# Kernel tuning notes

Measured on AMD Instinct MI355X. Metric: run time of the kernel, lower is better.

Reference implementation:

```python
import jax, jax.numpy as jnp
import numpy as np

NUM_LEVELS = 2
RADIUS = 3


def setup_inputs() -> dict:
    key = jax.random.key(0)
    k1, k2, k3 = jax.random.split(key, 3)
    x = jax.random.normal(k1, (4, 320, 9, 32, 32), dtype=jnp.float32)
    w_fc0 = jax.random.normal(k2, (160, 320), dtype=jnp.float32) * 0.05
    w_fc1 = jax.random.normal(k3, (160, 320), dtype=jnp.float32) * 0.05
    return {"x": x, "w_fc0": w_fc0, "w_fc1": w_fc1}


def _bilinear_zeros(img, xs, ys):
    # img: (M, H, W); xs, ys: (M, K) pixel coords.
    # Matches F.grid_sample(mode='bilinear', padding_mode='zeros', align_corners=True):
    # align_corners normalization round-trips to the raw pixel coords, and
    # out-of-bounds corners contribute zero.
    M, H, W = img.shape
    x0f = jnp.floor(xs)
    y0f = jnp.floor(ys)
    wx = xs - x0f
    wy = ys - y0f
    x0 = x0f.astype(jnp.int32)
    y0 = y0f.astype(jnp.int32)
    x1 = x0 + 1
    y1 = y0 + 1
    n = jnp.arange(M)[:, None]

    def corner(yi, xi):
        valid = (xi >= 0) & (xi < W) & (yi >= 0) & (yi < H)
        v = img[n, jnp.clip(yi, 0, H - 1), jnp.clip(xi, 0, W - 1)]
        return v * valid.astype(img.dtype)

    v00 = corner(y0, x0)
    v01 = corner(y0, x1)
    v10 = corner(y1, x0)
    v11 = corner(y1, x1)
    return (v00 * (1 - wx) * (1 - wy) + v01 * wx * (1 - wy)
            + v10 * (1 - wx) * wy + v11 * wx * wy)


def reference(x, w_fc0, w_fc1):
    b, c, T, h, w = x.shape
    xt = jnp.transpose(x, (0, 2, 1, 3, 4))  # (b, T, c, h, w)
    # 1x1 convs (no bias) on consecutive-frame pairs
    f0 = jnp.einsum('btchw,oc->bothw', xt[:, :-1], w_fc0)
    f1 = jnp.einsum('btchw,oc->bothw', xt[:, 1:], w_fc1)
    t = T - 1
    c2 = w_fc0.shape[0]
    f0 = f0.reshape(b * t, c2, h * w)
    f1 = f1.reshape(b * t, c2, h * w)
    # all-pairs correlation volume, normalized by channel count
    corr = jnp.einsum('nci,ncj->nij', f0, f1) / c2  # (bt, hw, hw)
    corr = corr.reshape(b * t * h * w, h, w)

    # pyramid via 2x2 avg pooling
    pyramid = [corr]
    for _ in range(NUM_LEVELS - 1):
        M, H, W = pyramid[-1].shape
        pyramid.append(pyramid[-1].reshape(M, H // 2, 2, W // 2, 2).mean(axis=(2, 4)))

    # per-pixel centroids (x, y), tiled over the bt batch axis
    ys, xs = jnp.meshgrid(jnp.arange(h), jnp.arange(w), indexing='ij')
    cx = jnp.tile(xs.reshape(-1).astype(jnp.float32), b * t)  # (bt*h*w,)
    cy = jnp.tile(ys.reshape(-1).astype(jnp.float32), b * t)

    # delta[i, j] = (d[i], d[j]); delta[...,0] -> x offset, delta[...,1] -> y offset
    r = RADIUS
    d = jnp.linspace(-r, r, 2 * r + 1)
    dx = jnp.repeat(d, 2 * r + 1)  # varies along first window dim
    dy = jnp.tile(d, 2 * r + 1)    # varies along second window dim

    outs = []
    for i, ci in enumerate(pyramid):
        xs_s = cx[:, None] / (2 ** i) + dx[None, :]  # (M, K)
        ys_s = cy[:, None] / (2 ** i) + dy[None, :]
        v = _bilinear_zeros(ci, xs_s, ys_s)          # (M, (2r+1)^2)
        outs.append(v.reshape(b * t, h, w, -1))
    out = jnp.concatenate(outs, axis=3)              # (bt, h, w, L*(2r+1)^2)
    out = out.reshape(b, t, h, w, -1)
    return jnp.transpose(out, (0, 4, 1, 2, 3)).astype(jnp.float32)
```

## Files before the change

kernel.cpp:

```cpp
#include <hip/hip_runtime.h>
#include <hip/hip_bf16.h>

typedef __attribute__((ext_vector_type(8))) short short8;
typedef __attribute__((ext_vector_type(4))) float f32x4;

static constexpr int HW = 1024;
static constexpr int C2 = 160;
static constexpr int FS = 168;
static constexpr int FSC = 160;
static constexpr int KSTEPS = 10;
static constexpr size_t PL = 32ull * 1024 * 160;
static constexpr size_t PPL = 32ull * 256 * 160;
static constexpr int AIMG = 6656;

__device__ inline short bfh(float v) {
  __hip_bfloat16 h = __float2bfloat16(v);
  return *reinterpret_cast<short*>(&h);
}
__device__ inline float bff(short s) {
  union { unsigned u; float f; } c;
  c.u = ((unsigned)(unsigned short)s) << 16;
  return c.f;
}

typedef const __attribute__((address_space(1))) void* gas_t;
typedef __attribute__((address_space(3))) void* las_t;
__device__ inline void gload_lds16(const void* g, void* l) {
  __builtin_amdgcn_global_load_lds((gas_t)g, (las_t)l, 16, 0, 0);
}

__global__ __launch_bounds__(256)
void wprep2_kernel(const float* __restrict__ w0, const float* __restrict__ w1,
                   short* __restrict__ wp) {
  const int id = blockIdx.x * 256 + threadIdx.x;
  if (id >= KSTEPS * 4 * AIMG) return;
  const int img = id / AIMG, r = id % AIMG;
  const int ks = img >> 2, qp = img & 3;
  short outv = 0;
  if (r < 6400) {
    const int hl = r / 3200;
    const int g2 = r % 3200;
    const int gr = g2 / 40, kk = g2 % 40;
    const int mat = gr >= 40;
    const int o = qp * 40 + gr - mat * 40;
    if (kk < 32) {
      const float v = (mat ? w1 : w0)[o * 320 + ks * 32 + kk];
      const short hb = bfh(v);
      outv = hl ? bfh(v - bff(hb)) : hb;
    }
  }
  wp[id] = outv;
}

__global__ __launch_bounds__(256)
void conv_fused(const float* __restrict__ x, const short* __restrict__ wprep2,
                short* __restrict__ f0bh, short* __restrict__ f0bl,
                short* __restrict__ f1bh, short* __restrict__ f1bl) {
  __shared__ __align__(16) char lds[31744];
  float* xF = reinterpret_cast<float*>(lds);
  short* aL = reinterpret_cast<short*>(lds + 18432);
  short* tL = reinterpret_cast<short*>(lds);

  const int flat = blockIdx.x;
  const int xcd = flat & 7;
  const int mem = (flat >> 3) & 7;
  const int qp = mem >> 1;
  const int pxh = mem & 1;
  const int g = (flat >> 6) * 8 + xcd;
  const int bb = g >> 5;
  const int pxt = (g & 31) * 2 + pxh;
  const int tid = threadIdx.x;
  const int lane = tid & 63;
  const int wave = __builtin_amdgcn_readfirstlane(tid >> 6);
  const int lr = lane & 15, kg = lane >> 4;

  f32x4 acc[5][3];
#pragma unroll
  for (int mt = 0; mt < 5; ++mt)
#pragma unroll
    for (int fi = 0; fi < 3; ++fi)
#pragma unroll
      for (int r = 0; r < 4; ++r) acc[mt][fi][r] = 0.f;

  const float* xg = x + ((size_t)(bb * 320) * 9) * 1024 + (size_t)pxt * 16;

  for (int ks = 0; ks < KSTEPS; ++ks) {
    if (ks) __syncthreads();
    {
      const short* src = wprep2 + (size_t)(ks * 4 + qp) * AIMG;
#pragma unroll
      for (int jj = 0; jj < 4; ++jj) {
        const int j = wave * 4 + jj;
        if (j < 13) gload_lds16(src + j * 512 + lane * 8, aL + j * 512);
      }
    }
#pragma unroll
    for (int jj = 0; jj < 5; ++jj) {
      const int gi = wave * 5 + jj;
      if (gi < 18) {
        const int f = gi >> 1, half = gi & 1;
        const int c = ks * 32 + half * 16 + (lane >> 2);
        const float* src = xg + ((size_t)c * 9 + f) * 1024 + (lane & 3) * 4;
        gload_lds16(src, xF + gi * 256);
      }
    }
    __syncthreads();

    short8 Ah[5], Al[5];
#pragma unroll
    for (int mt = 0; mt < 5; ++mt) {
      Ah[mt] = *reinterpret_cast<const short8*>(&aL[(mt * 16 + lr) * 40 + kg * 8]);
      Al[mt] = *reinterpret_cast<const short8*>(&aL[3200 + (mt * 16 + lr) * 40 + kg * 8]);
    }
#pragma unroll
    for (int fi = 0; fi < 3; ++fi) {
      const int f = wave + fi * 4;
      if (f < 9) {
        const float* bp = xF + f * 512 + kg * 128 + lr;
        float xv[8];
#pragma unroll
        for (int j = 0; j < 8; ++j) xv[j] = bp[j * 16];
        short8 Bh, Bl;
#pragma unroll
        for (int j = 0; j < 8; ++j) {
          const short h = bfh(xv[j]);
          Bh[j] = h;
          Bl[j] = bfh(xv[j] - bff(h));
        }
#pragma unroll
        for (int mt = 0; mt < 5; ++mt) {
          acc[mt][fi] = __builtin_amdgcn_mfma_f32_16x16x32_bf16(Ah[mt], Bh, acc[mt][fi], 0, 0, 0);
          acc[mt][fi] = __builtin_amdgcn_mfma_f32_16x16x32_bf16(Ah[mt], Bl, acc[mt][fi], 0, 0, 0);
          acc[mt][fi] = __builtin_amdgcn_mfma_f32_16x16x32_bf16(Al[mt], Bh, acc[mt][fi], 0, 0, 0);
        }
      }
    }
  }

#pragma unroll
  for (int m = 0; m < 2; ++m) {
    __syncthreads();
#pragma unroll
    for (int mt = 0; mt < 5; ++mt)
#pragma unroll
      for (int fi = 0; fi < 3; ++fi) {
        const int f = wave + fi * 4;
        const int tt = f - m;
        if (f < 9 && (unsigned)tt < 8u) {
#pragma unroll
          for (int rr = 0; rr < 4; ++rr) {
            const int gr = mt * 16 + kg * 4 + rr;
            if ((gr >= 40) == (m == 1)) {
              const int rowl = gr - m * 40;
              const int ql = rowl / 20, r20 = rowl % 20;
              const int c = 8 * r20 + tt;
              const int row = ql * 16 + lr;
              const float v = acc[mt][fi][rr];
              const short h = bfh(v);
              tL[row * FS + c] = h;
              tL[5376 + row * FS + c] = bfh(v - bff(h));
            }
          }
        }
      }
    __syncthreads();
#pragma unroll
    for (int i = 0; i < 5; ++i) {
      const int idx = tid + i * 256;
      const int plane = idx / 640, rem = idx % 640;
      const int row = rem / 20, c16 = rem % 20;
      const int ql = row >> 4, pxl = row & 15;
      const int n = bb * 8 + qp * 2 + ql;
      short* dst = (m == 0) ? (plane ? f0bl : f0bh) : (plane ? f1bl : f1bh);
      *reinterpret_cast<uint4*>(dst + ((size_t)n * 1024 + pxt * 16 + pxl) * 160 + c16 * 8) =
          *reinterpret_cast<const uint4*>(&tL[plane * 5376 + row * FS + c16 * 8]);
    }
  }
}

__global__ __launch_bounds__(256)
void pool_b(const short* __restrict__ f1bh, const short* __restrict__ f1bl,
            short* __restrict__ g1pbh, short* __restrict__ g1pbl) {
  const int id = blockIdx.x * 256 + threadIdx.x;
  if (id >= 32 * 256 * 20) return;
  const int c16 = id % 20;
  const int PX = (id / 20) & 255;
  const int n = id / (20 * 256);
  const int Y = PX >> 4, X = PX & 15;
  const int r0 = Y * 64 + X * 2;
  const size_t base = ((size_t)n * 1024 + r0) * 160 + c16 * 8;
  const short8 h00 = *reinterpret_cast<const short8*>(f1bh + base);
  const short8 h01 = *reinterpret_cast<const short8*>(f1bh + base + 160);
  const short8 h10 = *reinterpret_cast<const short8*>(f1bh + base + 32 * 160);
  const short8 h11 = *reinterpret_cast<const short8*>(f1bh + base + 33 * 160);
  const short8 l00 = *reinterpret_cast<const short8*>(f1bl + base);
  const short8 l01 = *reinterpret_cast<const short8*>(f1bl + base + 160);
  const short8 l10 = *reinterpret_cast<const short8*>(f1bl + base + 32 * 160);
  const short8 l11 = *reinterpret_cast<const short8*>(f1bl + base + 33 * 160);
  short8 ho, lo;
#pragma unroll
  for (int j = 0; j < 8; ++j) {
    const float v = 0.25f * ((bff(h00[j]) + bff(l00[j])) + (bff(h01[j]) + bff(l01[j])) +
                             (bff(h10[j]) + bff(l10[j])) + (bff(h11[j]) + bff(l11[j])));
    const short h = bfh(v);
    ho[j] = h;
    lo[j] = bfh(v - bff(h));
  }
  const size_t ob = ((size_t)n * 256 + PX) * 160 + c16 * 8;
  *reinterpret_cast<short8*>(g1pbh + ob) = ho;
  *reinterpret_cast<short8*>(g1pbl + ob) = lo;
}

__global__ __launch_bounds__(256)
void corr_kernel(const short* __restrict__ f0bh, const short* __restrict__ f0bl,
                 const short* __restrict__ f1bh, const short* __restrict__ f1bl,
                 const short* __restrict__ g1pbh, const short* __restrict__ g1pbl,
                 float* __restrict__ out) {
  __shared__ __align__(16) short f0L[2][32 * FSC];
  __shared__ __align__(16) short f1L[2][32 * FSC];
  __shared__ float S0[32 * 33];
  __shared__ float S1[2][32 * 17];
  const int flat = blockIdx.x;
  const int xcd = flat & 7;
  const int rr_ = flat >> 3;
  const int y = rr_ & 31;
  const int n = (xcd << 2) | (rr_ >> 5);
  const int bb = n >> 3, q = n & 7;
  const int tid = threadIdx.x;
  const int lane = tid & 63;
  const int wave = __builtin_amdgcn_readfirstlane(tid >> 6);
  const int lr = lane & 15, kg = lane >> 4;
  const int xx = tid & 31;
  const int hi = tid >> 5;
  const float inv = 1.f / 160.f;
  const size_t obase = (size_t)(bb * 784 + q) * 1024 + (size_t)y * 32;

  {
    const short* s0 = f0bh + ((size_t)n * 1024 + y * 32) * 160;
    const short* s1 = f0bl + ((size_t)n * 1024 + y * 32) * 160;
#pragma unroll
    for (int jj = 0; jj < 5; ++jj) {
      const int j = wave * 5 + jj;
      const int pl = j / 10, off = (j % 10) * 512;
      gload_lds16((pl ? s1 : s0) + off + lane * 8, &f0L[pl][off]);
    }
  }
  __syncthreads();

  const int mi0 = wave >> 1, ni0 = wave & 1;
  short8 a0h[5], a0l[5];
#pragma unroll
  for (int ks = 0; ks < 5; ++ks) {
    a0h[ks] = *reinterpret_cast<const short8*>(&f0L[0][(mi0 * 16 + lr) * FSC + ks * 32 + kg * 8]);
    a0l[ks] = *reinterpret_cast<const short8*>(&f0L[1][(mi0 * 16 + lr) * FSC + ks * 32 + kg * 8]);
  }

  for (int dyi = 0; dyi < 7; ++dyi) {
    const int yy = y + dyi - 3;
    const bool inr = (unsigned)yy < 32u;
    __syncthreads();
    if (inr) {
      const short* s0 = f1bh + ((size_t)n * 1024 + yy * 32) * 160;
      const short* s1 = f1bl + ((size_t)n * 1024 + yy * 32) * 160;
#pragma unroll
      for (int jj = 0; jj < 5; ++jj) {
        const int j = wave * 5 + jj;
        const int pl = j / 10, off = (j % 10) * 512;
        gload_lds16((pl ? s1 : s0) + off + lane * 8, &f1L[pl][off]);
      }
    }
    __syncthreads();
    if (inr) {
      f32x4 aA = {0.f, 0.f, 0.f, 0.f}, aB = aA, aC = aA;
#pragma unroll
      for (int ks = 0; ks < 5; ++ks) {
        const short8 bh = *reinterpret_cast<const short8*>(&f1L[0][(ni0 * 16 + lr) * FSC + ks * 32 + kg * 8]);
        const short8 bl = *reinterpret_cast<const short8*>(&f1L[1][(ni0 * 16 + lr) * FSC + ks * 32 + kg * 8]);
        aA = __builtin_amdgcn_mfma_f32_16x16x32_bf16(a0h[ks], bh, aA, 0, 0, 0);
        aB = __builtin_amdgcn_mfma_f32_16x16x32_bf16(a0h[ks], bl, aB, 0, 0, 0);
        aC = __builtin_amdgcn_mfma_f32_16x16x32_bf16(a0l[ks], bh, aC, 0, 0, 0);
      }
#pragma unroll
      for (int r = 0; r < 4; ++r)
        S0[(mi0 * 16 + kg * 4 + r) * 33 + ni0 * 16 + lr] = (aA[r] + aB[r]) + aC[r];
    }
    __syncthreads();
    if (hi < 7) {
      const int x2 = xx + hi - 3;
      const float val = (inr && (unsigned)x2 < 32u) ? S0[xx * 33 + x2] * inv : 0.f;
      out[obase + (size_t)(hi * 7 + dyi) * 8192 + xx] = val;
    }
  }

  short8 a1h[5], a1l[5];
  if (wave < 2) {
#pragma unroll
    for (int ks = 0; ks < 5; ++ks) {
      a1h[ks] = *reinterpret_cast<const short8*>(&f0L[0][(wave * 16 + lr) * FSC + ks * 32 + kg * 8]);
      a1l[ks] = *reinterpret_cast<const short8*>(&f0L[1][(wave * 16 + lr) * FSC + ks * 32 + kg * 8]);
    }
  }
  const int Y0 = (y >> 1) - 3;
  const float wy = (y & 1) ? 0.5f : 0.f;
  for (int v = 0; v < 8; ++v) {
    const int Y = Y0 + v;
    const bool inr = (unsigned)Y < 16u;
    __syncthreads();
    if (inr) {
      const short* s0 = g1pbh + ((size_t)n * 256 + Y * 16) * 160;
      const short* s1 = g1pbl + ((size_t)n * 256 + Y * 16) * 160;
#pragma unroll
      for (int jj = 0; jj < 3; ++jj) {
        const int j = wave * 3 + jj;
        if (j < 10) {
          const int pl = j / 5, off = (j % 5) * 512;
          gload_lds16((pl ? s1 : s0) + off + lane * 8, &f1L[pl][off]);
        }
      }
    }
    __syncthreads();
    if (wave < 2) {
      f32x4 aA = {0.f, 0.f, 0.f, 0.f}, aB = aA, aC = aA;
      if (inr) {
#pragma unroll
        for (int ks = 0; ks < 5; ++ks) {
          const short8 bh = *reinterpret_cast<const short8*>(&f1L[0][lr * FSC + ks * 32 + kg * 8]);
          const short8 bl = *reinterpret_cast<const short8*>(&f1L[1][lr * FSC + ks * 32 + kg * 8]);
          aA = __builtin_amdgcn_mfma_f32_16x16x32_bf16(a1h[ks], bh, aA, 0, 0, 0);
          aB = __builtin_amdgcn_mfma_f32_16x16x32_bf16(a1h[ks], bl, aB, 0, 0, 0);
          aC = __builtin_amdgcn_mfma_f32_16x16x32_bf16(a1l[ks], bh, aC, 0, 0, 0);
        }
      }
#pragma unroll
      for (int r = 0; r < 4; ++r)
        S1[v & 1][(wave * 16 + kg * 4 + r) * 17 + lr] = (aA[r] + aB[r]) + aC[r];
    }
    __syncthreads();
    if (v >= 1 && hi < 7) {
      const int dyi = v - 1;
      const int Xl = (xx >> 1) - 3 + hi;
      const int Xr = Xl + 1;
      const float* t0 = S1[(v - 1) & 1];
      const float* t1 = S1[v & 1];
      const float a00 = ((unsigned)Xl < 16u) ? t0[xx * 17 + Xl] : 0.f;
      const float a01 = ((unsigned)Xr < 16u) ? t0[xx * 17 + Xr] : 0.f;
      const float a10 = ((unsigned)Xl < 16u) ? t1[xx * 17 + Xl] : 0.f;
      const float a11 = ((unsigned)Xr < 16u) ? t1[xx * 17 + Xr] : 0.f;
      const float wx = (xx & 1) ? 0.5f : 0.f;
      const float val = ((1.f - wx) * ((1.f - wy) * a00 + wy * a10) +
                         wx * ((1.f - wy) * a01 + wy * a11)) * inv;
      out[obase + (size_t)(49 + hi * 7 + dyi) * 8192 + xx] = val;
    }
  }
}

extern "C" void kernel_launch(void* const* d_in, const int* in_sizes, int n_in,
                              void* d_out, int out_size, void* d_ws,
                              size_t ws_size, hipStream_t stream) {
  const float* x = (const float*)d_in[0];
  const float* w0 = (const float*)d_in[1];
  const float* w1 = (const float*)d_in[2];
  short* f0bh = (short*)d_ws;
  short* f0bl = f0bh + PL;
  short* f1bh = f0bl + PL;
  short* f1bl = f1bh + PL;
  short* g1pbh = f1bl + PL;
  short* g1pbl = g1pbh + PPL;
  short* wprep2 = g1pbh;
  float* out = (float*)d_out;

  wprep2_kernel<<<1040, 256, 0, stream>>>(w0, w1, wprep2);
  conv_fused<<<dim3(1024), 256, 0, stream>>>(x, wprep2, f0bh, f0bl, f1bh, f1bl);
  pool_b<<<640, 256, 0, stream>>>(f1bh, f1bl, g1pbh, g1pbl);
  corr_kernel<<<1024, 256, 0, stream>>>(f0bh, f0bl, f1bh, f1bl, g1pbh, g1pbl, out);
}
```

Measured before the change: 81.00 us.

## Double-buffer weight and input tiles in LDS for the fused conv

```diff
diff --git a/kernel.cpp b/kernel.cpp
--- a/kernel.cpp
+++ b/kernel.cpp
@@ -56,9 +56,9 @@
 void conv_fused(const float* __restrict__ x, const short* __restrict__ wprep2,
                 short* __restrict__ f0bh, short* __restrict__ f0bl,
                 short* __restrict__ f1bh, short* __restrict__ f1bl) {
-  __shared__ __align__(16) char lds[31744];
+  __shared__ __align__(16) char lds[63488];
   float* xF = reinterpret_cast<float*>(lds);
-  short* aL = reinterpret_cast<short*>(lds + 18432);
+  short* aL = reinterpret_cast<short*>(lds + 36864);
   short* tL = reinterpret_cast<short*>(lds);
 
   const int flat = blockIdx.x;
@@ -84,39 +84,46 @@
 
   const float* xg = x + ((size_t)(bb * 320) * 9) * 1024 + (size_t)pxt * 16;
 
+#define ISSUE(KS, BUF)                                                        \
+  {                                                                           \
+    const short* asrc = wprep2 + (size_t)((KS) * 4 + qp) * AIMG;              \
+    _Pragma("unroll") for (int jj = 0; jj < 4; ++jj) {                        \
+      const int j = wave * 4 + jj;                                            \
+      if (j < 13)                                                             \
+        gload_lds16(asrc + j * 512 + lane * 8, aL + (BUF) * AIMG + j * 512);  \
+    }                                                                         \
+    _Pragma("unroll") for (int jj = 0; jj < 5; ++jj) {                        \
+      const int gi = wave * 5 + jj;                                           \
+      if (gi < 18) {                                                          \
+        const int f_ = gi >> 1, half_ = gi & 1;                               \
+        const int c_ = (KS) * 32 + half_ * 16 + (lane >> 2);                  \
+        gload_lds16(xg + ((size_t)c_ * 9 + f_) * 1024 + (lane & 3) * 4,       \
+                    xF + (BUF) * 4608 + gi * 256);                            \
+      }                                                                       \
+    }                                                                         \
+  }
+
+  ISSUE(0, 0);
+
+#pragma unroll
   for (int ks = 0; ks < KSTEPS; ++ks) {
-    if (ks) __syncthreads();
-    {
-      const short* src = wprep2 + (size_t)(ks * 4 + qp) * AIMG;
-#pragma unroll
-      for (int jj = 0; jj < 4; ++jj) {
-        const int j = wave * 4 + jj;
-        if (j < 13) gload_lds16(src + j * 512 + lane * 8, aL + j * 512);
-      }
-    }
-#pragma unroll
-    for (int jj = 0; jj < 5; ++jj) {
-      const int gi = wave * 5 + jj;
-      if (gi < 18) {
-        const int f = gi >> 1, half = gi & 1;
-        const int c = ks * 32 + half * 16 + (lane >> 2);
-        const float* src = xg + ((size_t)c * 9 + f) * 1024 + (lane & 3) * 4;
-        gload_lds16(src, xF + gi * 256);
-      }
-    }
-    __syncthreads();
-
+    const int buf = ks & 1;
+    __syncthreads();
+    if (ks + 1 < KSTEPS) ISSUE(ks + 1, buf ^ 1);
+
+    const short* aB = aL + buf * AIMG;
+    const float* xB = xF + buf * 4608;
     short8 Ah[5], Al[5];
 #pragma unroll
     for (int mt = 0; mt < 5; ++mt) {
-      Ah[mt] = *reinterpret_cast<const short8*>(&aL[(mt * 16 + lr) * 40 + kg * 8]);
-      Al[mt] = *reinterpret_cast<const short8*>(&aL[3200 + (mt * 16 + lr) * 40 + kg * 8]);
+      Ah[mt] = *reinterpret_cast<const short8*>(&aB[(mt * 16 + lr) * 40 + kg * 8]);
+      Al[mt] = *reinterpret_cast<const short8*>(&aB[3200 + (mt * 16 + lr) * 40 + kg * 8]);
     }
 #pragma unroll
     for (int fi = 0; fi < 3; ++fi) {
       const int f = wave + fi * 4;
       if (f < 9) {
-        const float* bp = xF + f * 512 + kg * 128 + lr;
+        const float* bp = xB + f * 512 + kg * 128 + lr;
         float xv[8];
 #pragma unroll
         for (int j = 0; j < 8; ++j) xv[j] = bp[j * 16];
@@ -136,6 +143,7 @@
       }
     }
   }
+#undef ISSUE
 
 #pragma unroll
   for (int m = 0; m < 2; ++m) {
```

Result: slower. 84.30 us (+4.1%).
